# Kernel tuning notes

Measured on AMD Instinct MI355X. Metric: run time of the kernel, lower is better.

## Reference

```python
import jax, jax.numpy as jnp
import numpy as np

N, K, T = 100000, 12, 365
PERIODS = (0.25, 0.5, 1.0, 2.0)
TWO_PI = 2.0 * np.pi


def _smooth_amplitude(param, idx, w, sf):
    # param: [N], idx: [N,K], w: [N,K]
    neigh = param[idx]                                   # gather [N,K]
    wavg = jnp.sum(neigh * w, axis=1)                    # [N]
    var = jnp.var(neigh, axis=1, ddof=1)                 # torch.var unbiased
    af = sf / (1.0 + var * 0.1)
    return (1.0 - af) * param + af * wavg


def _smooth_phase(param, idx, w, sf):
    cur_re, cur_im = jnp.cos(param), jnp.sin(param)      # unit complex, split re/im
    neigh = param[idx]                                   # [N,K]
    wav_re = jnp.sum(jnp.cos(neigh) * w, axis=1)
    wav_im = jnp.sum(jnp.sin(neigh) * w, axis=1)
    consistency = jnp.sqrt(wav_re * wav_re + wav_im * wav_im)
    af = sf * consistency
    mix_re = (1.0 - af) * cur_re + af * wav_re
    mix_im = (1.0 - af) * cur_im + af * wav_im
    return jnp.arctan2(mix_im, mix_re)                   # torch.angle


def setup_inputs() -> dict:
    key = jax.random.key(0)
    ks = jax.random.split(key, 6)
    time_vector = (jnp.arange(T, dtype=jnp.float32) / 365.25)
    constant_offset = jax.random.normal(ks[0], (N,), dtype=jnp.float32)
    linear_trend = jax.random.normal(ks[1], (N,), dtype=jnp.float32)  # ps00_rates buffer
    seasonal_amplitudes = jax.random.uniform(ks[2], (N, 4), dtype=jnp.float32) * 4.0
    seasonal_phases = jax.random.uniform(ks[3], (N, 4), dtype=jnp.float32) * TWO_PI
    neighbor_indices = jax.random.randint(ks[4], (N, K), 0, N, dtype=jnp.int32)
    w = jax.random.uniform(ks[5], (N, K), dtype=jnp.float32) + 1e-3
    neighbor_weights = w / jnp.sum(w, axis=1, keepdims=True)  # row-normalized like _compute_enhanced_weights
    return {
        'time_vector': time_vector,
        'constant_offset': constant_offset,
        'linear_trend': linear_trend,
        'seasonal_amplitudes': seasonal_amplitudes,
        'seasonal_phases': seasonal_phases,
        'neighbor_weights': neighbor_weights,
        'neighbor_indices': neighbor_indices,
    }


def reference(time_vector, constant_offset, linear_trend, seasonal_amplitudes,
              seasonal_phases, neighbor_weights, neighbor_indices):
    t = time_vector[None, :]                              # [1,T]
    signals = constant_offset[:, None] + linear_trend[:, None] * t  # [N,T]
    for i, period in enumerate(PERIODS):
        amp = _smooth_amplitude(seasonal_amplitudes[:, i], neighbor_indices,
                                neighbor_weights, 0.25)
        ph = _smooth_phase(seasonal_phases[:, i], neighbor_indices,
                           neighbor_weights, 0.15)
        freq = 1.0 / period
        signals = signals + amp[:, None] * jnp.sin(TWO_PI * freq * t + ph[:, None])
    return signals
```

## Files before the change

### kernel.cpp

```cpp
#include <hip/hip_runtime.h>

#define N_PTS 100000
#define KNB   12
#define TLEN  365
#define FUSED_ROWS 64
#define SYNTH_ROWS 16
#define PARAMS_BYTES ((size_t)N_PTS * 12 * sizeof(float))


__device__ __forceinline__ float bf2f(unsigned short u) {
    return __uint_as_float(((unsigned int)u) << 16);
}
__device__ __forceinline__ unsigned short f2bf(float f) {
    unsigned int x = __float_as_uint(f);
    unsigned int r = (x + 0x7FFFu + ((x >> 16) & 1u)) >> 16;
    return (unsigned short)r;
}

__device__ __forceinline__ bool detect_bf16(const void* tvec) {
    return ((const unsigned int*)tvec)[0] != 0u;
}

__device__ __forceinline__ float ld(const void* p, size_t i, bool b16) {
    if (b16) return bf2f(((const unsigned short*)p)[i]);
    return ((const float*)p)[i];
}

__device__ void compute_params(
    int n, bool b16,
    const void* __restrict__ amps,
    const void* __restrict__ phs,
    const void* __restrict__ wgts,
    const int*  __restrict__ idx,
    const void* __restrict__ coff,
    const void* __restrict__ trend,
    float outp[12])
{
    float sx[4]  = {0,0,0,0}, sxx[4] = {0,0,0,0}, swx[4] = {0,0,0,0};
    float wre[4] = {0,0,0,0}, wim[4] = {0,0,0,0};

    #pragma unroll
    for (int k = 0; k < KNB; ++k) {
        int j = idx[(size_t)n * KNB + k];
        j = (j < 0) ? 0 : ((j >= N_PTS) ? N_PTS - 1 : j);
        float wk = ld(wgts, (size_t)n * KNB + k, b16);
        #pragma unroll
        for (int i = 0; i < 4; ++i) {
            float a = ld(amps, (size_t)j * 4 + i, b16);
            float p = ld(phs,  (size_t)j * 4 + i, b16);
            sx[i]  += a;
            sxx[i] += a * a;
            swx[i] += wk * a;
            float s, c;
            __sincosf(p, &s, &c);
            wre[i] += wk * c;
            wim[i] += wk * s;
        }
    }

    outp[0] = ld(coff,  n, b16);
    outp[1] = ld(trend, n, b16);
    #pragma unroll
    for (int i = 0; i < 4; ++i) {
        float aof = ld(amps, (size_t)n * 4 + i, b16);
        float pof = ld(phs,  (size_t)n * 4 + i, b16);

        float mean  = sx[i] * (1.0f / KNB);
        float var   = fmaxf((sxx[i] - (float)KNB * mean * mean) * (1.0f / (KNB - 1)), 0.0f);
        float afa   = 0.25f / (1.0f + 0.1f * var);
        float amp_s = (1.0f - afa) * aof + afa * swx[i];

        float cons = sqrtf(wre[i] * wre[i] + wim[i] * wim[i]);
        float afp  = 0.15f * cons;
        float s, c;
        __sincosf(pof, &s, &c);
        float mre = (1.0f - afp) * c + afp * wre[i];
        float mim = (1.0f - afp) * s + afp * wim[i];
        float h   = sqrtf(mre * mre + mim * mim);
        float ai, bi;
        if (h > 1e-30f) {
            float scale = amp_s / h;
            ai = mre * scale;
            bi = mim * scale;
        } else {
            ai = amp_s;
            bi = 0.0f;
        }
        outp[2 + i] = ai;
        outp[6 + i] = bi;
    }
}

__device__ __forceinline__ void synth_row_store(
    void* out, size_t o, float v, bool b16)
{
    if (b16) ((unsigned short*)out)[o] = f2bf(v);
    else     ((float*)out)[o] = v;
}


__global__ __launch_bounds__(256) void smooth_kernel(
    const void* __restrict__ amps,
    const void* __restrict__ phs,
    const void* __restrict__ wgts,
    const int*  __restrict__ idx,
    const void* __restrict__ coff,
    const void* __restrict__ trend,
    const void* __restrict__ tvec,
    float*      __restrict__ params)
{
    int n = blockIdx.x * blockDim.x + threadIdx.x;
    if (n >= N_PTS) return;
    bool b16 = detect_bf16(tvec);
    float outp[12];
    compute_params(n, b16, amps, phs, wgts, idx, coff, trend, outp);
    #pragma unroll
    for (int i = 0; i < 12; ++i) params[(size_t)n * 12 + i] = outp[i];
}

__global__ __launch_bounds__(384) void synth_kernel(
    const float* __restrict__ params,
    const void*  __restrict__ tvec,
    void*        __restrict__ out)
{
    bool b16 = detect_bf16(tvec);
    int t = threadIdx.x;
    if (t >= TLEN) return;
    float tval = ld(tvec, t, b16);

    const float W0 = 25.132741228718345f;
    const float W1 = 12.566370614359172f;
    const float W2 = 6.283185307179586f;
    const float W3 = 3.141592653589793f;
    float s0, c0, s1, c1, s2, c2, s3, c3;
    __sincosf(W0 * tval, &s0, &c0);
    __sincosf(W1 * tval, &s1, &c1);
    __sincosf(W2 * tval, &s2, &c2);
    __sincosf(W3 * tval, &s3, &c3);

    int row0 = blockIdx.x * SYNTH_ROWS;
    int rend = min(row0 + SYNTH_ROWS, N_PTS);
    for (int n = row0; n < rend; ++n) {
        const float* p = params + (size_t)n * 12;
        float v = fmaf(p[1], tval, p[0]);
        v = fmaf(p[2], s0, v);
        v = fmaf(p[3], s1, v);
        v = fmaf(p[4], s2, v);
        v = fmaf(p[5], s3, v);
        v = fmaf(p[6], c0, v);
        v = fmaf(p[7], c1, v);
        v = fmaf(p[8], c2, v);
        v = fmaf(p[9], c3, v);
        synth_row_store(out, (size_t)n * TLEN + t, v, b16);
    }
}


__global__ __launch_bounds__(384) void fused_kernel(
    const void* __restrict__ amps,
    const void* __restrict__ phs,
    const void* __restrict__ wgts,
    const int*  __restrict__ idx,
    const void* __restrict__ coff,
    const void* __restrict__ trend,
    const void* __restrict__ tvec,
    void*       __restrict__ out)
{
    __shared__ float P[FUSED_ROWS][12];
    bool b16 = detect_bf16(tvec);

    int row0 = blockIdx.x * FUSED_ROWS;
    int tid  = threadIdx.x;

    if (tid < FUSED_ROWS) {
        int n = row0 + tid;
        if (n < N_PTS) {
            float outp[12];
            compute_params(n, b16, amps, phs, wgts, idx, coff, trend, outp);
            #pragma unroll
            for (int i = 0; i < 12; ++i) P[tid][i] = outp[i];
        }
    }
    __syncthreads();

    int t = tid;
    if (t >= TLEN) return;
    float tval = ld(tvec, t, b16);

    const float W0 = 25.132741228718345f;
    const float W1 = 12.566370614359172f;
    const float W2 = 6.283185307179586f;
    const float W3 = 3.141592653589793f;
    float s0, c0, s1, c1, s2, c2, s3, c3;
    __sincosf(W0 * tval, &s0, &c0);
    __sincosf(W1 * tval, &s1, &c1);
    __sincosf(W2 * tval, &s2, &c2);
    __sincosf(W3 * tval, &s3, &c3);

    int rend = min(row0 + FUSED_ROWS, N_PTS);
    for (int n = row0; n < rend; ++n) {
        int r = n - row0;
        float v = fmaf(P[r][1], tval, P[r][0]);
        v = fmaf(P[r][2], s0, v);
        v = fmaf(P[r][3], s1, v);
        v = fmaf(P[r][4], s2, v);
        v = fmaf(P[r][5], s3, v);
        v = fmaf(P[r][6], c0, v);
        v = fmaf(P[r][7], c1, v);
        v = fmaf(P[r][8], c2, v);
        v = fmaf(P[r][9], c3, v);
        synth_row_store(out, (size_t)n * TLEN + t, v, b16);
    }
}

extern "C" void kernel_launch(void* const* d_in, const int* in_sizes, int n_in,
                              void* d_out, int out_size, void* d_ws, size_t ws_size,
                              hipStream_t stream) {
    const void* tvec  = d_in[0];
    const void* coff  = d_in[1];
    const void* trend = d_in[2];
    const void* amps  = d_in[3];
    const void* phs   = d_in[4];
    const void* wgts  = d_in[5];
    const int*  idx   = (const int*)d_in[6];

    if (d_ws != nullptr && ws_size >= PARAMS_BYTES) {
        float* params = (float*)d_ws;
        smooth_kernel<<<(N_PTS + 255) / 256, 256, 0, stream>>>(
            amps, phs, wgts, idx, coff, trend, tvec, params);
        int sblk = (N_PTS + SYNTH_ROWS - 1) / SYNTH_ROWS;
        synth_kernel<<<sblk, 384, 0, stream>>>(params, tvec, d_out);
    } else {
        int fblk = (N_PTS + FUSED_ROWS - 1) / FUSED_ROWS;
        fused_kernel<<<fblk, 384, 0, stream>>>(
            amps, phs, wgts, idx, coff, trend, tvec, d_out);
    }
}
```

Before: 224.9 us.

## Fuse smoothing and synthesis into single 64-thread kernel with full-wave param compute

Replaces the two-kernel path (smooth into workspace, then synthesize) with one fused kernel of 64 threads per block. Every thread computes one row's parameters, so the whole wave is busy, and then loops over 6 time columns per thread to write the output rows. This removes the workspace round-trip and the second launch, and drops the old fused design where most threads sat idle during the gather phase. In exchange it adds register pressure from the per-column sincos arrays and gives narrow blocks with low per-block write parallelism. The output is a 146 MB fp32 write, so the kernel stays bound by store bandwidth.

```diff
diff --git a/kernel.cpp b/kernel.cpp
--- a/kernel.cpp
+++ b/kernel.cpp
@@ -99,6 +99,78 @@
 }
 
 
+#define NCOL 6
+
+__global__ __launch_bounds__(64) void fused64_kernel(
+    const void* __restrict__ amps,
+    const void* __restrict__ phs,
+    const void* __restrict__ wgts,
+    const int*  __restrict__ idx,
+    const void* __restrict__ coff,
+    const void* __restrict__ trend,
+    const void* __restrict__ tvec,
+    void*       __restrict__ out)
+{
+    __shared__ float P[FUSED_ROWS][12];
+    bool b16 = detect_bf16(tvec);
+
+    int row0 = blockIdx.x * FUSED_ROWS;
+    int tid  = threadIdx.x;
+
+    int n = row0 + tid;
+    if (n < N_PTS) {
+        float outp[12];
+        compute_params(n, b16, amps, phs, wgts, idx, coff, trend, outp);
+        #pragma unroll
+        for (int i = 0; i < 12; ++i) P[tid][i] = outp[i];
+    }
+    __syncthreads();
+
+    const float W0 = 25.132741228718345f;
+    const float W1 = 12.566370614359172f;
+    const float W2 = 6.283185307179586f;
+    const float W3 = 3.141592653589793f;
+
+    float tv[NCOL];
+    float s0[NCOL], c0[NCOL], s1[NCOL], c1[NCOL];
+    float s2[NCOL], c2[NCOL], s3[NCOL], c3[NCOL];
+    #pragma unroll
+    for (int c = 0; c < NCOL; ++c) {
+        int t = tid + 64 * c;
+        float tval = (t < TLEN) ? ld(tvec, t, b16) : 0.0f;
+        tv[c] = tval;
+        __sincosf(W0 * tval, &s0[c], &c0[c]);
+        __sincosf(W1 * tval, &s1[c], &c1[c]);
+        __sincosf(W2 * tval, &s2[c], &c2[c]);
+        __sincosf(W3 * tval, &s3[c], &c3[c]);
+    }
+
+    int rend = min(row0 + FUSED_ROWS, N_PTS) - row0;
+    for (int r = 0; r < rend; ++r) {
+        float p0 = P[r][0], p1 = P[r][1];
+        float p2 = P[r][2], p3 = P[r][3], p4 = P[r][4], p5 = P[r][5];
+        float p6 = P[r][6], p7 = P[r][7], p8 = P[r][8], p9 = P[r][9];
+        size_t base = (size_t)(row0 + r) * TLEN;
+        #pragma unroll
+        for (int c = 0; c < NCOL; ++c) {
+            int t = tid + 64 * c;
+            if (t < TLEN) {
+                float v = fmaf(p1, tv[c], p0);
+                v = fmaf(p2, s0[c], v);
+                v = fmaf(p3, s1[c], v);
+                v = fmaf(p4, s2[c], v);
+                v = fmaf(p5, s3[c], v);
+                v = fmaf(p6, c0[c], v);
+                v = fmaf(p7, c1[c], v);
+                v = fmaf(p8, c2[c], v);
+                v = fmaf(p9, c3[c], v);
+                synth_row_store(out, base + t, v, b16);
+            }
+        }
+    }
+}
+
+
 __global__ __launch_bounds__(256) void smooth_kernel(
     const void* __restrict__ amps,
     const void* __restrict__ phs,
@@ -155,64 +227,6 @@
     }
 }
 
-
-__global__ __launch_bounds__(384) void fused_kernel(
-    const void* __restrict__ amps,
-    const void* __restrict__ phs,
-    const void* __restrict__ wgts,
-    const int*  __restrict__ idx,
-    const void* __restrict__ coff,
-    const void* __restrict__ trend,
-    const void* __restrict__ tvec,
-    void*       __restrict__ out)
-{
-    __shared__ float P[FUSED_ROWS][12];
-    bool b16 = detect_bf16(tvec);
-
-    int row0 = blockIdx.x * FUSED_ROWS;
-    int tid  = threadIdx.x;
-
-    if (tid < FUSED_ROWS) {
-        int n = row0 + tid;
-        if (n < N_PTS) {
-            float outp[12];
-            compute_params(n, b16, amps, phs, wgts, idx, coff, trend, outp);
-            #pragma unroll
-            for (int i = 0; i < 12; ++i) P[tid][i] = outp[i];
-        }
-    }
-    __syncthreads();
-
-    int t = tid;
-    if (t >= TLEN) return;
-    float tval = ld(tvec, t, b16);
-
-    const float W0 = 25.132741228718345f;
-    const float W1 = 12.566370614359172f;
-    const float W2 = 6.283185307179586f;
-    const float W3 = 3.141592653589793f;
-    float s0, c0, s1, c1, s2, c2, s3, c3;
-    __sincosf(W0 * tval, &s0, &c0);
-    __sincosf(W1 * tval, &s1, &c1);
-    __sincosf(W2 * tval, &s2, &c2);
-    __sincosf(W3 * tval, &s3, &c3);
-
-    int rend = min(row0 + FUSED_ROWS, N_PTS);
-    for (int n = row0; n < rend; ++n) {
-        int r = n - row0;
-        float v = fmaf(P[r][1], tval, P[r][0]);
-        v = fmaf(P[r][2], s0, v);
-        v = fmaf(P[r][3], s1, v);
-        v = fmaf(P[r][4], s2, v);
-        v = fmaf(P[r][5], s3, v);
-        v = fmaf(P[r][6], c0, v);
-        v = fmaf(P[r][7], c1, v);
-        v = fmaf(P[r][8], c2, v);
-        v = fmaf(P[r][9], c3, v);
-        synth_row_store(out, (size_t)n * TLEN + t, v, b16);
-    }
-}
-
 extern "C" void kernel_launch(void* const* d_in, const int* in_sizes, int n_in,
                               void* d_out, int out_size, void* d_ws, size_t ws_size,
                               hipStream_t stream) {
@@ -224,15 +238,7 @@
     const void* wgts  = d_in[5];
     const int*  idx   = (const int*)d_in[6];
 
-    if (d_ws != nullptr && ws_size >= PARAMS_BYTES) {
-        float* params = (float*)d_ws;
-        smooth_kernel<<<(N_PTS + 255) / 256, 256, 0, stream>>>(
-            amps, phs, wgts, idx, coff, trend, tvec, params);
-        int sblk = (N_PTS + SYNTH_ROWS - 1) / SYNTH_ROWS;
-        synth_kernel<<<sblk, 384, 0, stream>>>(params, tvec, d_out);
-    } else {
-        int fblk = (N_PTS + FUSED_ROWS - 1) / FUSED_ROWS;
-        fused_kernel<<<fblk, 384, 0, stream>>>(
-            amps, phs, wgts, idx, coff, trend, tvec, d_out);
-    }
-}
+    int fblk = (N_PTS + FUSED_ROWS - 1) / FUSED_ROWS;
+    fused64_kernel<<<fblk, 64, 0, stream>>>(
+        amps, phs, wgts, idx, coff, trend, tvec, d_out);
+}
```

Result: no change. 223.5 us (-0.6%).
